# Optimization experiments

Measured on AMD Instinct MI355X. Metric: run time of the kernel, lower is better.

## Reference

```python
import jax, jax.numpy as jnp
import numpy as np

DIM = 1024
HEADS = 16
HEAD_DIM = DIM // HEADS
SCALE = HEAD_DIM ** -0.5


def setup_inputs() -> dict:
    key = jax.random.key(0)
    k1, k2, k3, k4 = jax.random.split(key, 4)
    x = jax.random.normal(k1, (2, 2048, DIM), dtype=jnp.float32)
    # nn.Linear(dim, 3*dim, bias=False): weight shape (3*dim, dim), y = x @ W.T
    w_qkv = jax.random.normal(k2, (3 * DIM, DIM), dtype=jnp.float32) * (DIM ** -0.5)
    w_proj = jax.random.normal(k3, (DIM, DIM), dtype=jnp.float32) * (DIM ** -0.5)
    head_w = jnp.ones((HEADS,), dtype=jnp.float32)
    return {"x": x, "w_qkv": w_qkv, "w_proj": w_proj, "head_w": head_w}


def reference(x, w_qkv, w_proj, head_w) -> jnp.ndarray:
    B, N, C = x.shape
    qkv = jnp.einsum("bnc,dc->bnd", x, w_qkv)  # [B,N,3C]
    qkv = qkv.reshape(B, N, 3, HEADS, HEAD_DIM).transpose(2, 0, 3, 1, 4)
    q, k, v = qkv[0], qkv[1], qkv[2]  # each [B,H,N,Dh]
    attn = jnp.einsum("bhqd,bhkd->bhqk", q, k) * SCALE  # [B,H,N,N]
    attn = jax.nn.softmax(attn, axis=-1)
    out = jnp.einsum("bhqk,bhkd->bhqd", attn, v)  # [B,H,N,Dh]
    hw = jax.nn.softmax(head_w)[None, :, None, None]
    out = out * hw
    out = out.transpose(0, 2, 1, 3).reshape(B, N, C)
    return jnp.einsum("bnc,dc->bnd", out, w_proj)
```

## Files before the change

### kernel.cpp

```cpp
#include <hip/hip_runtime.h>

typedef _Float16 half_t;
typedef _Float16 half8 __attribute__((ext_vector_type(8)));
typedef _Float16 half4_t __attribute__((ext_vector_type(4)));
typedef float floatx4 __attribute__((ext_vector_type(4)));
typedef float floatx16 __attribute__((ext_vector_type(16)));

#define B_SZ 2
#define SEQ 2048
#define DIM_ 1024
#define NH 16
#define DH 64
#define ROWS (B_SZ * SEQ)

__device__ __forceinline__ void gl2lds16(const void* g, void* l) {
  __builtin_amdgcn_global_load_lds((const __attribute__((address_space(1))) unsigned int*)g,
                                   (__attribute__((address_space(3))) unsigned int*)l, 16, 0, 0);
}

__global__ __launch_bounds__(256) void convert_all(const float4* __restrict__ x,
                                                   const float4* __restrict__ wq,
                                                   const float4* __restrict__ wp,
                                                   half4_t* __restrict__ dst,
                                                   int nx, int nq, int np) {
  int i = blockIdx.x * blockDim.x + threadIdx.x;
  float4 v;
  if (i < nx) v = x[i];
  else if (i < nx + nq) v = wq[i - nx];
  else if (i < nx + nq + np) v = wp[i - nx - nq];
  else return;
  half4_t h;
  h.x = (half_t)v.x; h.y = (half_t)v.y; h.z = (half_t)v.z; h.w = (half_t)v.w;
  dst[i] = h;
}

template <int MODE, int BN>
__global__ __launch_bounds__(256) void gemm32(const half_t* __restrict__ A,
                                              const half_t* __restrict__ Bt,
                                              half_t* __restrict__ q16,
                                              half_t* __restrict__ k16,
                                              half_t* __restrict__ vT16,
                                              float* __restrict__ outp) {
  constexpr int K = 1024;
  constexpr int NT = BN / 64;
  __shared__ __align__(16) half_t a_lds[128 * 64];
  __shared__ __align__(16) half_t b_lds[BN * 64];
  const int t = threadIdx.x;
  const int wave = t >> 6, lane = t & 63;
  const int l31 = lane & 31, hw = lane >> 5;
  const int wm = wave >> 1, wn = wave & 1;
  const int row0 = blockIdx.y * 128, col0 = blockIdx.x * BN;

  floatx16 acc[2][NT];
#pragma unroll
  for (int i = 0; i < 2; ++i)
#pragma unroll
    for (int j = 0; j < NT; ++j)
#pragma unroll
      for (int r = 0; r < 16; ++r) acc[i][j][r] = 0.f;

  for (int k0 = 0; k0 < K; k0 += 64) {
#pragma unroll
    for (int hi = 0; hi < 4; ++hi) {
      int s = t + hi * 256;
      int row = s >> 3, c = s & 7;
      int sc = c ^ (row & 7);
      gl2lds16(A + (size_t)(row0 + row) * K + (k0 + sc * 8), a_lds + (wave * 64 + hi * 256) * 8);
    }
#pragma unroll
    for (int hi = 0; hi < BN / 32; ++hi) {
      int s = t + hi * 256;
      int row = s >> 3, c = s & 7;
      int sc = c ^ (row & 7);
      gl2lds16(Bt + (size_t)(col0 + row) * K + (k0 + sc * 8), b_lds + (wave * 64 + hi * 256) * 8);
    }
    __syncthreads();
    half8 af[2][4], bf[NT][4];
#pragma unroll
    for (int mt = 0; mt < 2; ++mt) {
      int row = wm * 64 + mt * 32 + l31;
#pragma unroll
      for (int kf = 0; kf < 4; ++kf)
        af[mt][kf] = *(const half8*)(a_lds + row * 64 + ((kf * 2 + hw) ^ (row & 7)) * 8);
    }
#pragma unroll
    for (int nt = 0; nt < NT; ++nt) {
      int row = wn * (BN / 2) + nt * 32 + l31;
#pragma unroll
      for (int kf = 0; kf < 4; ++kf)
        bf[nt][kf] = *(const half8*)(b_lds + row * 64 + ((kf * 2 + hw) ^ (row & 7)) * 8);
    }
#pragma unroll
    for (int kf = 0; kf < 4; ++kf)
#pragma unroll
      for (int mt = 0; mt < 2; ++mt)
#pragma unroll
        for (int nt = 0; nt < NT; ++nt)
          acc[mt][nt] =
              __builtin_amdgcn_mfma_f32_32x32x16_f16(af[mt][kf], bf[nt][kf], acc[mt][nt], 0, 0, 0);
    __syncthreads();
  }

  if (MODE == 0) {
    const int which = col0 >> 10;
#pragma unroll
    for (int mt = 0; mt < 2; ++mt)
#pragma unroll
      for (int nt = 0; nt < NT; ++nt) {
        int growb = row0 + wm * 64 + mt * 32;
        int gcol = col0 + wn * (BN / 2) + nt * 32 + l31;
        int hc = gcol & 1023, h = hc >> 6, d = hc & 63;
        if (which == 2) {
#pragma unroll
          for (int rq = 0; rq < 4; ++rq) {
            int grow = growb + 8 * rq + 4 * hw;
            int b = grow >> 11, n0 = grow & 2047;
            int bh = b * NH + h;
            half4_t h4;
            h4.x = (half_t)acc[mt][nt][rq * 4 + 0];
            h4.y = (half_t)acc[mt][nt][rq * 4 + 1];
            h4.z = (half_t)acc[mt][nt][rq * 4 + 2];
            h4.w = (half_t)acc[mt][nt][rq * 4 + 3];
            *(half4_t*)(vT16 + ((size_t)bh * DH + d) * SEQ + n0) = h4;
          }
        } else {
#pragma unroll
          for (int r = 0; r < 16; ++r) {
            int grow = growb + (r & 3) + 8 * (r >> 2) + 4 * hw;
            int b = grow >> 11, n = grow & 2047;
            int bh = b * NH + h;
            float v = acc[mt][nt][r];
            if (which == 0)
              q16[((size_t)bh * SEQ + n) * DH + d] = (half_t)(v * 0.125f);
            else
              k16[((size_t)bh * SEQ + n) * DH + d] = (half_t)v;
          }
        }
      }
  } else {
#pragma unroll
    for (int mt = 0; mt < 2; ++mt)
#pragma unroll
      for (int nt = 0; nt < NT; ++nt) {
        int growb = row0 + wm * 64 + mt * 32;
        int gcol = col0 + wn * (BN / 2) + nt * 32 + l31;
#pragma unroll
        for (int r = 0; r < 16; ++r) {
          int grow = growb + (r & 3) + 8 * (r >> 2) + 4 * hw;
          outp[(size_t)grow * DIM_ + gcol] = acc[mt][nt][r];
        }
      }
  }
}

__global__ __launch_bounds__(256) void attn_p1(const half_t* __restrict__ q16,
                                               const half_t* __restrict__ k16,
                                               const half_t* __restrict__ vT16,
                                               half_t* __restrict__ opart,
                                               float* __restrict__ psums) {
  __shared__ __align__(16) half_t k_lds[2][64 * 64];
  __shared__ __align__(16) half_t v_lds[2][64 * 64];

  const int t = threadIdx.x;
  const int wave = t >> 6, lane = t & 63;
  const int l15 = lane & 15, quad = lane >> 4;
  const int blk = blockIdx.x;
  const int js = blk & 1, qt = (blk >> 1) & 15, bh = blk >> 5;
  const half_t* qp = q16 + (size_t)bh * SEQ * DH;
  const half_t* kp = k16 + (size_t)bh * SEQ * DH;
  const half_t* vp = vT16 + (size_t)bh * DH * SEQ;
  const int q0w = qt * 128 + wave * 32;
  const int jbase = js * 1024;

  const int s0 = t, s1 = t + 256;
  const int r0_ = s0 >> 3, c0_ = (s0 & 7) ^ (r0_ & 7);
  const int r1_ = s1 >> 3, c1_ = (s1 & 7) ^ (r1_ & 7);

  half8 qf[2][2];
#pragma unroll
  for (int mi = 0; mi < 2; ++mi)
#pragma unroll
    for (int kf = 0; kf < 2; ++kf)
      qf[mi][kf] = *(const half8*)(qp + (size_t)(q0w + mi * 16 + l15) * DH + kf * 32 + quad * 8);

  const floatx4 z4 = {0.f, 0.f, 0.f, 0.f};
  floatx4 o[2][4];
  float psum[2] = {0.f, 0.f};
#pragma unroll
  for (int mi = 0; mi < 2; ++mi)
#pragma unroll
    for (int i = 0; i < 4; ++i) o[mi][i] = z4;

  gl2lds16(kp + (size_t)(jbase + r0_) * DH + c0_ * 8, &k_lds[0][(wave * 64) * 8]);
  gl2lds16(vp + (size_t)r0_ * SEQ + jbase + c0_ * 8, &v_lds[0][(wave * 64) * 8]);
  gl2lds16(kp + (size_t)(jbase + r1_) * DH + c1_ * 8, &k_lds[0][(wave * 64 + 256) * 8]);
  gl2lds16(vp + (size_t)r1_ * SEQ + jbase + c1_ * 8, &v_lds[0][(wave * 64 + 256) * 8]);

  int cur = 0;
  for (int jt = 0; jt < 16; ++jt) {
    __syncthreads();

    if (jt + 1 < 16) {
      const int j0 = jbase + (jt + 1) * 64, nb = cur ^ 1;
      gl2lds16(kp + (size_t)(j0 + r0_) * DH + c0_ * 8, &k_lds[nb][(wave * 64) * 8]);
      gl2lds16(vp + (size_t)r0_ * SEQ + j0 + c0_ * 8, &v_lds[nb][(wave * 64) * 8]);
      gl2lds16(kp + (size_t)(j0 + r1_) * DH + c1_ * 8, &k_lds[nb][(wave * 64 + 256) * 8]);
      gl2lds16(vp + (size_t)r1_ * SEQ + j0 + c1_ * 8, &v_lds[nb][(wave * 64 + 256) * 8]);
    }

    const half_t* kl = k_lds[cur];
    const half_t* vl = v_lds[cur];

    floatx4 st[2][4];
#pragma unroll
    for (int mi = 0; mi < 2; ++mi)
#pragma unroll
      for (int nt = 0; nt < 4; ++nt) st[mi][nt] = z4;
#pragma unroll
    for (int kf = 0; kf < 2; ++kf)
#pragma unroll
      for (int nt = 0; nt < 4; ++nt) {
        int row = nt * 16 + l15;
        half8 kb = *(const half8*)(kl + row * 64 + (((kf << 2) | quad) ^ (row & 7)) * 8);
        st[0][nt] = __builtin_amdgcn_mfma_f32_16x16x32_f16(kb, qf[0][kf], st[0][nt], 0, 0, 0);
        st[1][nt] = __builtin_amdgcn_mfma_f32_16x16x32_f16(kb, qf[1][kf], st[1][nt], 0, 0, 0);
      }

    half4_t pf[2][4];
#pragma unroll
    for (int mi = 0; mi < 2; ++mi)
#pragma unroll
      for (int nt = 0; nt < 4; ++nt) {
        float p0 = __expf(st[mi][nt][0]);
        float p1 = __expf(st[mi][nt][1]);
        float p2 = __expf(st[mi][nt][2]);
        float p3 = __expf(st[mi][nt][3]);
        psum[mi] += (p0 + p1) + (p2 + p3);
        half4_t pk;
        pk.x = (half_t)p0; pk.y = (half_t)p1; pk.z = (half_t)p2; pk.w = (half_t)p3;
        pf[mi][nt] = pk;
      }

#pragma unroll
    for (int jt2 = 0; jt2 < 4; ++jt2)
#pragma unroll
      for (int dt = 0; dt < 4; ++dt) {
        int row = dt * 16 + l15;
        int ch = (jt2 * 2 + (quad >> 1)) ^ (l15 & 7);
        half4_t vb = *(const half4_t*)(vl + row * 64 + ch * 8 + (quad & 1) * 4);
        o[0][dt] = __builtin_amdgcn_mfma_f32_16x16x16f16(pf[0][jt2], vb, o[0][dt], 0, 0, 0);
        o[1][dt] = __builtin_amdgcn_mfma_f32_16x16x16f16(pf[1][jt2], vb, o[1][dt], 0, 0, 0);
      }
    cur ^= 1;
  }

#pragma unroll
  for (int mi = 0; mi < 2; ++mi) {
    psum[mi] += __shfl_xor(psum[mi], 16, 64);
    psum[mi] += __shfl_xor(psum[mi], 32, 64);
  }
  if (quad == 0) {
#pragma unroll
    for (int mi = 0; mi < 2; ++mi)
      psums[((size_t)(js * 32 + bh)) * SEQ + q0w + mi * 16 + l15] = psum[mi];
  }

#pragma unroll
  for (int mi = 0; mi < 2; ++mi)
#pragma unroll
    for (int r = 0; r < 4; ++r) {
      int n = q0w + mi * 16 + quad * 4 + r;
      size_t base = ((size_t)(js * 32 + bh) * SEQ + n) * DH;
#pragma unroll
      for (int dt = 0; dt < 4; ++dt)
        opart[base + dt * 16 + l15] = (half_t)o[mi][dt][r];
    }
}

__global__ __launch_bounds__(256) void combine(const half_t* __restrict__ opart,
                                               const float* __restrict__ psums,
                                               const float* __restrict__ head_w,
                                               half_t* __restrict__ attn16) {
  int idx = blockIdx.x * blockDim.x + threadIdx.x;
  int d4 = idx & 15, n = (idx >> 4) & 2047, bh = idx >> 15;
  int h = bh & 15, b = bh >> 4;
  const size_t jstr = (size_t)32 * SEQ * DH;
  size_t off = ((size_t)bh * SEQ + n) * DH + d4 * 4;
  half4_t o0 = *(const half4_t*)(opart + off);
  half4_t o1 = *(const half4_t*)(opart + jstr + off);
  float ps = psums[(size_t)bh * SEQ + n] + psums[(size_t)32 * SEQ + (size_t)bh * SEQ + n];

  float mw = head_w[0];
#pragma unroll
  for (int i = 1; i < NH; ++i) mw = fmaxf(mw, head_w[i]);
  float sw = 0.f;
#pragma unroll
  for (int i = 0; i < NH; ++i) sw += __expf(head_w[i] - mw);
  float hwv = __expf(head_w[h] - mw) / sw;

  float scl = hwv / ps;
  half4_t r;
  r.x = (half_t)(((float)o0.x + (float)o1.x) * scl);
  r.y = (half_t)(((float)o0.y + (float)o1.y) * scl);
  r.z = (half_t)(((float)o0.z + (float)o1.z) * scl);
  r.w = (half_t)(((float)o0.w + (float)o1.w) * scl);
  *(half4_t*)(attn16 + ((size_t)(b * SEQ + n)) * DIM_ + h * DH + d4 * 4) = r;
}

extern "C" void kernel_launch(void* const* d_in, const int* in_sizes, int n_in,
                              void* d_out, int out_size, void* d_ws, size_t ws_size,
                              hipStream_t stream) {
  const float* x = (const float*)d_in[0];
  const float* w_qkv = (const float*)d_in[1];
  const float* w_proj = (const float*)d_in[2];
  const float* head_w = (const float*)d_in[3];
  float* out = (float*)d_out;

  half_t* x16 = (half_t*)d_ws;
  half_t* wq16 = x16 + (size_t)ROWS * DIM_;
  half_t* wp16 = wq16 + (size_t)3 * DIM_ * DIM_;
  half_t* q16 = wp16 + (size_t)DIM_ * DIM_;
  half_t* k16 = q16 + (size_t)ROWS * DIM_;
  half_t* vT16 = k16 + (size_t)ROWS * DIM_;
  half_t* attn16 = vT16 + (size_t)ROWS * DIM_;
  half_t* opart = attn16 + (size_t)ROWS * DIM_;
  float* psums = (float*)(opart + (size_t)2 * 32 * SEQ * DH);

  const int nx = ROWS * DIM_ / 4, nq = 3 * DIM_ * DIM_ / 4, np = DIM_ * DIM_ / 4;
  convert_all<<<(nx + nq + np) / 256, 256, 0, stream>>>((const float4*)x, (const float4*)w_qkv,
                                                        (const float4*)w_proj, (half4_t*)x16,
                                                        nx, nq, np);

  gemm32<0, 128><<<dim3(24, 32), 256, 0, stream>>>(x16, wq16, q16, k16, vT16, nullptr);
  attn_p1<<<32 * 16 * 2, 256, 0, stream>>>(q16, k16, vT16, opart, psums);
  combine<<<(32 * SEQ * DH / 4) / 256, 256, 0, stream>>>(opart, psums, head_w, attn16);
  gemm32<1, 64><<<dim3(16, 32), 256, 0, stream>>>(attn16, wp16, nullptr, nullptr, nullptr, out);
}
```

Before: 193.5 us.

## Double-buffer GEMM LDS with BK=32 and interleave attention QK/exp per tile

The GEMM kernel now uses a two-stage LDS ring with K-step 32, prefetching the next slice via global_load_lds while computing the current one. This removes the second barrier per iteration and keeps total LDS size unchanged. Launch-bound occupancy hints are added to both kernels (3 blocks for GEMM, 4 for attention). The attention S computation is reordered so exp and packing follow each column tile's MFMAs, lowering live registers. The risks are register spills under the tighter bounds and more loop iterations from the halved K step.

```diff
diff --git a/kernel.cpp b/kernel.cpp
--- a/kernel.cpp
+++ b/kernel.cpp
@@ -35,16 +35,17 @@
 }
 
 template <int MODE, int BN>
-__global__ __launch_bounds__(256) void gemm32(const half_t* __restrict__ A,
-                                              const half_t* __restrict__ Bt,
-                                              half_t* __restrict__ q16,
-                                              half_t* __restrict__ k16,
-                                              half_t* __restrict__ vT16,
-                                              float* __restrict__ outp) {
+__global__ __launch_bounds__(256, 3) void gemm32(const half_t* __restrict__ A,
+                                                 const half_t* __restrict__ Bt,
+                                                 half_t* __restrict__ q16,
+                                                 half_t* __restrict__ k16,
+                                                 half_t* __restrict__ vT16,
+                                                 float* __restrict__ outp) {
   constexpr int K = 1024;
+  constexpr int BK = 32;
   constexpr int NT = BN / 64;
-  __shared__ __align__(16) half_t a_lds[128 * 64];
-  __shared__ __align__(16) half_t b_lds[BN * 64];
+  __shared__ __align__(16) half_t a_lds[2][128 * BK];
+  __shared__ __align__(16) half_t b_lds[2][BN * BK];
   const int t = threadIdx.x;
   const int wave = t >> 6, lane = t & 63;
   const int l31 = lane & 31, hw = lane >> 5;
@@ -59,46 +60,51 @@
 #pragma unroll
       for (int r = 0; r < 16; ++r) acc[i][j][r] = 0.f;
 
-  for (int k0 = 0; k0 < K; k0 += 64) {
-#pragma unroll
-    for (int hi = 0; hi < 4; ++hi) {
+  auto stage = [&](int buf, int k0) {
+#pragma unroll
+    for (int hi = 0; hi < 2; ++hi) {
       int s = t + hi * 256;
-      int row = s >> 3, c = s & 7;
-      int sc = c ^ (row & 7);
-      gl2lds16(A + (size_t)(row0 + row) * K + (k0 + sc * 8), a_lds + (wave * 64 + hi * 256) * 8);
-    }
-#pragma unroll
-    for (int hi = 0; hi < BN / 32; ++hi) {
+      int row = s >> 2, c = s & 3;
+      int sc = c ^ ((row >> 1) & 3);
+      gl2lds16(A + (size_t)(row0 + row) * K + (k0 + sc * 8),
+               &a_lds[buf][(wave * 64 + hi * 256) * 8]);
+    }
+#pragma unroll
+    for (int hi = 0; hi < BN / 64; ++hi) {
       int s = t + hi * 256;
-      int row = s >> 3, c = s & 7;
-      int sc = c ^ (row & 7);
-      gl2lds16(Bt + (size_t)(col0 + row) * K + (k0 + sc * 8), b_lds + (wave * 64 + hi * 256) * 8);
-    }
+      int row = s >> 2, c = s & 3;
+      int sc = c ^ ((row >> 1) & 3);
+      gl2lds16(Bt + (size_t)(col0 + row) * K + (k0 + sc * 8),
+               &b_lds[buf][(wave * 64 + hi * 256) * 8]);
+    }
+  };
+
+  stage(0, 0);
+  int cur = 0;
+  for (int k0 = 0; k0 < K; k0 += BK) {
     __syncthreads();
-    half8 af[2][4], bf[NT][4];
-#pragma unroll
-    for (int mt = 0; mt < 2; ++mt) {
-      int row = wm * 64 + mt * 32 + l31;
-#pragma unroll
-      for (int kf = 0; kf < 4; ++kf)
-        af[mt][kf] = *(const half8*)(a_lds + row * 64 + ((kf * 2 + hw) ^ (row & 7)) * 8);
-    }
-#pragma unroll
-    for (int nt = 0; nt < NT; ++nt) {
-      int row = wn * (BN / 2) + nt * 32 + l31;
-#pragma unroll
-      for (int kf = 0; kf < 4; ++kf)
-        bf[nt][kf] = *(const half8*)(b_lds + row * 64 + ((kf * 2 + hw) ^ (row & 7)) * 8);
-    }
-#pragma unroll
-    for (int kf = 0; kf < 4; ++kf)
+    if (k0 + BK < K) stage(cur ^ 1, k0 + BK);
+
+#pragma unroll
+    for (int kf = 0; kf < 2; ++kf) {
+      half8 af[2], bf[NT];
+#pragma unroll
+      for (int mt = 0; mt < 2; ++mt) {
+        int row = wm * 64 + mt * 32 + l31;
+        af[mt] = *(const half8*)(&a_lds[cur][row * BK + (((kf << 1) | hw) ^ ((row >> 1) & 3)) * 8]);
+      }
+#pragma unroll
+      for (int nt = 0; nt < NT; ++nt) {
+        int row = wn * (BN / 2) + nt * 32 + l31;
+        bf[nt] = *(const half8*)(&b_lds[cur][row * BK + (((kf << 1) | hw) ^ ((row >> 1) & 3)) * 8]);
+      }
 #pragma unroll
       for (int mt = 0; mt < 2; ++mt)
 #pragma unroll
         for (int nt = 0; nt < NT; ++nt)
-          acc[mt][nt] =
-              __builtin_amdgcn_mfma_f32_32x32x16_f16(af[mt][kf], bf[nt][kf], acc[mt][nt], 0, 0, 0);
-    __syncthreads();
+          acc[mt][nt] = __builtin_amdgcn_mfma_f32_32x32x16_f16(af[mt], bf[nt], acc[mt][nt], 0, 0, 0);
+    }
+    cur ^= 1;
   }
 
   if (MODE == 0) {
@@ -153,11 +159,11 @@
   }
 }
 
-__global__ __launch_bounds__(256) void attn_p1(const half_t* __restrict__ q16,
-                                               const half_t* __restrict__ k16,
-                                               const half_t* __restrict__ vT16,
-                                               half_t* __restrict__ opart,
-                                               float* __restrict__ psums) {
+__global__ __launch_bounds__(256, 4) void attn_p1(const half_t* __restrict__ q16,
+                                                  const half_t* __restrict__ k16,
+                                                  const half_t* __restrict__ vT16,
+                                                  half_t* __restrict__ opart,
+                                                  float* __restrict__ psums) {
   __shared__ __align__(16) half_t k_lds[2][64 * 64];
   __shared__ __align__(16) half_t v_lds[2][64 * 64];
 
@@ -211,35 +217,34 @@
     const half_t* kl = k_lds[cur];
     const half_t* vl = v_lds[cur];
 
-    floatx4 st[2][4];
-#pragma unroll
-    for (int mi = 0; mi < 2; ++mi)
-#pragma unroll
-      for (int nt = 0; nt < 4; ++nt) st[mi][nt] = z4;
-#pragma unroll
-    for (int kf = 0; kf < 2; ++kf)
-#pragma unroll
-      for (int nt = 0; nt < 4; ++nt) {
-        int row = nt * 16 + l15;
+    half4_t pf[2][4];
+#pragma unroll
+    for (int nt = 0; nt < 4; ++nt) {
+      int row = nt * 16 + l15;
+      floatx4 st0 = z4, st1 = z4;
+#pragma unroll
+      for (int kf = 0; kf < 2; ++kf) {
         half8 kb = *(const half8*)(kl + row * 64 + (((kf << 2) | quad) ^ (row & 7)) * 8);
-        st[0][nt] = __builtin_amdgcn_mfma_f32_16x16x32_f16(kb, qf[0][kf], st[0][nt], 0, 0, 0);
-        st[1][nt] = __builtin_amdgcn_mfma_f32_16x16x32_f16(kb, qf[1][kf], st[1][nt], 0, 0, 0);
-      }
-
-    half4_t pf[2][4];
-#pragma unroll
-    for (int mi = 0; mi < 2; ++mi)
-#pragma unroll
-      for (int nt = 0; nt < 4; ++nt) {
-        float p0 = __expf(st[mi][nt][0]);
-        float p1 = __expf(st[mi][nt][1]);
-        float p2 = __expf(st[mi][nt][2]);
-        float p3 = __expf(st[mi][nt][3]);
-        psum[mi] += (p0 + p1) + (p2 + p3);
+        st0 = __builtin_amdgcn_mfma_f32_16x16x32_f16(kb, qf[0][kf], st0, 0, 0, 0);
+        st1 = __builtin_amdgcn_mfma_f32_16x16x32_f16(kb, qf[1][kf], st1, 0, 0, 0);
+      }
+      {
+        float p0 = __expf(st0[0]), p1 = __expf(st0[1]);
+        float p2 = __expf(st0[2]), p3 = __expf(st0[3]);
+        psum[0] += (p0 + p1) + (p2 + p3);
         half4_t pk;
         pk.x = (half_t)p0; pk.y = (half_t)p1; pk.z = (half_t)p2; pk.w = (half_t)p3;
-        pf[mi][nt] = pk;
-      }
+        pf[0][nt] = pk;
+      }
+      {
+        float p0 = __expf(st1[0]), p1 = __expf(st1[1]);
+        float p2 = __expf(st1[2]), p3 = __expf(st1[3]);
+        psum[1] += (p0 + p1) + (p2 + p3);
+        half4_t pk;
+        pk.x = (half_t)p0; pk.y = (half_t)p1; pk.z = (half_t)p2; pk.w = (half_t)p3;
+        pf[1][nt] = pk;
+      }
+    }
 
 #pragma unroll
     for (int jt2 = 0; jt2 < 4; ++jt2)
```

After: 198.5 us. 1.03x slower.
